# Optimization experiments

Measured on AMD Instinct MI355X. Metric: run time of the kernel, lower is better.

The kernel has to match this reference:

```python
import jax, jax.numpy as jnp
import numpy as np

EMBED = 1024
HEADS = 16
HEAD_DIM = EMBED // HEADS
HIDDEN = 4 * EMBED
EPS = 1e-5


def layer_norm(x, g, b):
    mu = jnp.mean(x, axis=-1, keepdims=True)
    var = jnp.var(x, axis=-1, keepdims=True)
    return (x - mu) * jax.lax.rsqrt(var + EPS) * g + b


def setup_inputs() -> dict:
    key = jax.random.key(0)
    ks = jax.random.split(key, 12)
    s_e = 1.0 / np.sqrt(EMBED)
    s_h = 1.0 / np.sqrt(HIDDEN)
    return {
        "x": jax.random.normal(ks[0], (8, 1024, EMBED), dtype=jnp.float32),
        "ln1_g": jnp.ones((EMBED,), jnp.float32),
        "ln1_b": jnp.zeros((EMBED,), jnp.float32),
        "w_qkv": jax.random.normal(ks[1], (EMBED, 3 * EMBED), jnp.float32) * s_e,
        "b_qkv": jax.random.normal(ks[2], (3 * EMBED,), jnp.float32) * s_e,
        "w_out": jax.random.normal(ks[3], (EMBED, EMBED), jnp.float32) * s_e,
        "b_out": jax.random.normal(ks[4], (EMBED,), jnp.float32) * s_e,
        "ln2_g": jnp.ones((EMBED,), jnp.float32),
        "ln2_b": jnp.zeros((EMBED,), jnp.float32),
        "w_up": jax.random.normal(ks[5], (EMBED, HIDDEN), jnp.float32) * s_e,
        "b_up": jax.random.normal(ks[6], (HIDDEN,), jnp.float32) * s_e,
        "w_down": jax.random.normal(ks[7], (HIDDEN, EMBED), jnp.float32) * s_h,
        "b_down": jax.random.normal(ks[8], (EMBED,), jnp.float32) * s_h,
    }


def reference(x, ln1_g, ln1_b, w_qkv, b_qkv, w_out, b_out,
              ln2_g, ln2_b, w_up, b_up, w_down, b_down):
    B, T, C = x.shape
    # --- attention sub-block ---
    h = layer_norm(x, ln1_g, ln1_b)
    qkv = h @ w_qkv + b_qkv                                   # [B,T,3C]
    q, k, v = jnp.split(qkv, 3, axis=-1)
    def heads(t):  # [B,T,C] -> [B,H,T,D]
        return t.reshape(B, T, HEADS, HEAD_DIM).transpose(0, 2, 1, 3)
    q, k, v = heads(q), heads(k), heads(v)
    scale = HEAD_DIM ** -0.5
    attn = jax.nn.softmax(jnp.einsum('bhqd,bhkd->bhqk', q, k) * scale, axis=-1)
    y = jnp.einsum('bhqk,bhkd->bhqd', attn, v)                # [B,H,T,D]
    y = y.transpose(0, 2, 1, 3).reshape(B, T, C)
    x = x + y @ w_out + b_out
    # --- MLP sub-block ---
    h = layer_norm(x, ln2_g, ln2_b)
    h = jax.nn.relu(h @ w_up + b_up)
    x = x + h @ w_down + b_down
    return x
```

## Files before the change

kernel.cpp:

```cpp
#include <hip/hip_runtime.h>
#include <stdint.h>


typedef __attribute__((ext_vector_type(8))) short short8;
typedef __attribute__((ext_vector_type(4))) short short4v;
typedef __attribute__((ext_vector_type(4))) float floatx4;

#define NROWS 8192

__device__ __forceinline__ unsigned short f2bf(float f) {
    union { float f; unsigned u; } x; x.f = f;
    unsigned r = x.u + 0x7fffu + ((x.u >> 16) & 1u);
    return (unsigned short)(r >> 16);
}
__device__ __forceinline__ float bf2f(unsigned short h) {
    union { unsigned u; float f; } x; x.u = (unsigned)h << 16; return x.f;
}

__device__ __forceinline__ void gl2lds16(const unsigned short* g, unsigned short* l) {
    __builtin_amdgcn_global_load_lds(
        (const __attribute__((address_space(1))) unsigned int*)(uintptr_t)g,
        (__attribute__((address_space(3))) unsigned int*)(unsigned int)(uintptr_t)l,
        16, 0, 0);
}

__global__ __launch_bounds__(256) void prep_kernel(
    const float* __restrict__ w_qkv, const float* __restrict__ w_out,
    const float* __restrict__ w_up, const float* __restrict__ w_down,
    unsigned short* __restrict__ wqkvT, unsigned short* __restrict__ woutT,
    unsigned short* __restrict__ wupT, unsigned short* __restrict__ wdownT,
    const float* __restrict__ x, const float* __restrict__ g,
    const float* __restrict__ b, unsigned short* __restrict__ h1)
{
    int bid = blockIdx.x;
    __shared__ unsigned short tile[32][33];
    __shared__ float rs[4], rs2[4];
    if (bid < 12288) {
        const float* in; unsigned short* out; int K, N, nb, tb;
        if (bid < 3072)      { in = w_qkv;  out = wqkvT;  K = 1024; N = 3072; nb = 96;  tb = bid; }
        else if (bid < 4096) { in = w_out;  out = woutT;  K = 1024; N = 1024; nb = 32;  tb = bid - 3072; }
        else if (bid < 8192) { in = w_up;   out = wupT;   K = 1024; N = 4096; nb = 128; tb = bid - 4096; }
        else                 { in = w_down; out = wdownT; K = 4096; N = 1024; nb = 32;  tb = bid - 8192; }
        int n0 = (tb % nb) * 32, k0 = (tb / nb) * 32;
        int tx = threadIdx.x & 31, ty = threadIdx.x >> 5;
        #pragma unroll
        for (int i = 0; i < 4; ++i)
            tile[ty + i * 8][tx] = f2bf(in[(size_t)(k0 + ty + i * 8) * N + n0 + tx]);
        __syncthreads();
        #pragma unroll
        for (int i = 0; i < 4; ++i)
            out[(size_t)(n0 + ty + i * 8) * K + k0 + tx] = tile[tx][ty + i * 8];
    } else {
        int row = bid - 12288, t = threadIdx.x;
        const float4* xr = (const float4*)(x + (size_t)row * 1024);
        float4 v = xr[t];
        float s  = v.x + v.y + v.z + v.w;
        float s2 = v.x * v.x + v.y * v.y + v.z * v.z + v.w * v.w;
        #pragma unroll
        for (int off = 32; off; off >>= 1) {
            s  += __shfl_xor(s,  off, 64);
            s2 += __shfl_xor(s2, off, 64);
        }
        int w = t >> 6;
        if ((t & 63) == 0) { rs[w] = s; rs2[w] = s2; }
        __syncthreads();
        s  = rs[0] + rs[1] + rs[2] + rs[3];
        s2 = rs2[0] + rs2[1] + rs2[2] + rs2[3];
        float mean = s * (1.0f / 1024.0f);
        float var  = s2 * (1.0f / 1024.0f) - mean * mean;
        float rstd = rsqrtf(var + 1e-5f);
        float4 gv = ((const float4*)g)[t];
        float4 bv = ((const float4*)b)[t];
        ushort4 o;
        o.x = f2bf((v.x - mean) * rstd * gv.x + bv.x);
        o.y = f2bf((v.y - mean) * rstd * gv.y + bv.y);
        o.z = f2bf((v.z - mean) * rstd * gv.z + bv.z);
        o.w = f2bf((v.w - mean) * rstd * gv.w + bv.w);
        ((ushort4*)(h1 + (size_t)row * 1024))[t] = o;
    }
}

__global__ __launch_bounds__(256) void ln_bf16b(
    const unsigned short* __restrict__ x, const float* __restrict__ g,
    const float* __restrict__ b, unsigned short* __restrict__ out)
{
    int row = blockIdx.x, t = threadIdx.x;
    ushort4 hv = ((const ushort4*)(x + (size_t)row * 1024))[t];
    float v0 = bf2f(hv.x), v1 = bf2f(hv.y), v2 = bf2f(hv.z), v3 = bf2f(hv.w);
    float s  = v0 + v1 + v2 + v3;
    float s2 = v0 * v0 + v1 * v1 + v2 * v2 + v3 * v3;
    #pragma unroll
    for (int off = 32; off; off >>= 1) {
        s  += __shfl_xor(s,  off, 64);
        s2 += __shfl_xor(s2, off, 64);
    }
    __shared__ float rs[4], rs2[4];
    int w = t >> 6;
    if ((t & 63) == 0) { rs[w] = s; rs2[w] = s2; }
    __syncthreads();
    s  = rs[0] + rs[1] + rs[2] + rs[3];
    s2 = rs2[0] + rs2[1] + rs2[2] + rs2[3];
    float mean = s * (1.0f / 1024.0f);
    float var  = s2 * (1.0f / 1024.0f) - mean * mean;
    float rstd = rsqrtf(var + 1e-5f);
    float4 gv = ((const float4*)g)[t];
    float4 bv = ((const float4*)b)[t];
    ushort4 o;
    o.x = f2bf((v0 - mean) * rstd * gv.x + bv.x);
    o.y = f2bf((v1 - mean) * rstd * gv.y + bv.y);
    o.z = f2bf((v2 - mean) * rstd * gv.z + bv.z);
    o.w = f2bf((v3 - mean) * rstd * gv.w + bv.w);
    ((ushort4*)(out + (size_t)row * 1024))[t] = o;
}

template <int MODE>
__global__ __launch_bounds__(512, 2) void gemm_8ph(
    const unsigned short* __restrict__ A, const unsigned short* __restrict__ Bt,
    int M, int N, int K,
    const float* __restrict__ bias,
    unsigned short* __restrict__ outB)
{
    int m0 = blockIdx.x * 256, n0 = blockIdx.y * 256;
    int tid = threadIdx.x;
    int w = tid >> 6, l = tid & 63, quad = l >> 4, lr = l & 15;
    int wm = w >> 2, wn = w & 3;

    __shared__ unsigned short As[2][256 * 64];
    __shared__ unsigned short Bs[2][256 * 64];

    floatx4 acc[8][4];
    #pragma unroll
    for (int i = 0; i < 8; ++i)
        #pragma unroll
        for (int j = 0; j < 4; ++j)
            acc[i][j] = (floatx4){0.f, 0.f, 0.f, 0.f};

    int srow = l >> 3;
    int swz  = ((l & 7) ^ srow) * 8;
    int arow1 = (w < 4) ? 16 * w : 128 + 16 * (w - 4);
    const unsigned short* Ag = A  + (size_t)(m0 + arow1 + srow) * K + swz;
    const unsigned short* Bg = Bt + (size_t)(n0 + 16 * w + srow) * K + swz;
    int nt = K >> 6;

    auto SB = [&](unsigned short* dst, int h, int kt) {
        #pragma unroll
        for (int u = 0; u < 2; ++u)
            gl2lds16(Bg + (size_t)(128 * h + 8 * u) * K + kt * 64,
                     &dst[(128 * h + 16 * w + 8 * u) * 64]);
    };
    auto SA1 = [&](unsigned short* dst, int kt) {
        #pragma unroll
        for (int u = 0; u < 2; ++u)
            gl2lds16(Ag + (size_t)(8 * u) * K + kt * 64,
                     &dst[(arow1 + 8 * u) * 64]);
    };
    auto SA2 = [&](unsigned short* dst, int kt) {
        #pragma unroll
        for (int u = 0; u < 2; ++u)
            gl2lds16(Ag + (size_t)(64 + 8 * u) * K + kt * 64,
                     &dst[(arow1 + 64 + 8 * u) * 64]);
    };

    SB(Bs[0], 0, 0); SB(Bs[0], 1, 0); SA1(As[0], 0); SA2(As[0], 0);
    SB(Bs[1], 0, 1); SB(Bs[1], 1, 1); SA1(As[1], 1);
    asm volatile("s_waitcnt vmcnt(6)" ::: "memory");
    __builtin_amdgcn_s_barrier();

    for (int t = 0; t < nt; ++t) {
        int b = t & 1;
        const unsigned short* Asb = As[b];
        const unsigned short* Bsb = Bs[b];
        short8 bfr[4][2];
        #pragma unroll
        for (int p = 0; p < 4; ++p) {
            if (p == 0)      { if (t + 1 < nt) SA2(As[b ^ 1], t + 1); }
            else if (p == 1) { if (t + 2 < nt) SB(Bs[b], 0, t + 2); }
            else if (p == 2) { if (t + 2 < nt) SB(Bs[b], 1, t + 2); }
            else             { if (t + 2 < nt) SA1(As[b], t + 2); }

            if (p == 0) {
                #pragma unroll
                for (int j = 0; j < 4; ++j)
                    #pragma unroll
                    for (int s = 0; s < 2; ++s)
                        bfr[j][s] = *(const short8*)
                            &Bsb[(64 * wn + 16 * j + lr) * 64 +
                                 (((s * 4 + quad) ^ (lr & 7)) * 8)];
            }
            short8 af[2][2];
            #pragma unroll
            for (int i = 0; i < 2; ++i)
                #pragma unroll
                for (int s = 0; s < 2; ++s)
                    af[i][s] = *(const short8*)
                        &Asb[(128 * wm + 32 * p + 16 * i + lr) * 64 +
                             (((s * 4 + quad) ^ (lr & 7)) * 8)];

            __builtin_amdgcn_s_barrier();
            asm volatile("s_waitcnt lgkmcnt(0)" ::: "memory");
            __builtin_amdgcn_s_setprio(1);
            #pragma unroll
            for (int i = 0; i < 2; ++i)
                #pragma unroll
                for (int j = 0; j < 4; ++j) {
                    acc[2 * p + i][j] = __builtin_amdgcn_mfma_f32_16x16x32_bf16(
                        af[i][0], bfr[j][0], acc[2 * p + i][j], 0, 0, 0);
                    acc[2 * p + i][j] = __builtin_amdgcn_mfma_f32_16x16x32_bf16(
                        af[i][1], bfr[j][1], acc[2 * p + i][j], 0, 0, 0);
                }
            __builtin_amdgcn_s_setprio(0);
            if (p == 3) {
                if (t + 2 >= nt) asm volatile("s_waitcnt vmcnt(0)" ::: "memory");
                else             asm volatile("s_waitcnt vmcnt(6)" ::: "memory");
            }
            __builtin_amdgcn_s_barrier();
        }
    }

    #pragma unroll
    for (int mi = 0; mi < 8; ++mi)
        #pragma unroll
        for (int j = 0; j < 4; ++j)
            #pragma unroll
            for (int r = 0; r < 4; ++r) {
                int m = m0 + 128 * wm + 16 * mi + quad * 4 + r;
                int n = n0 + 64 * wn + 16 * j + lr;
                outB[(size_t)m * N + n] = f2bf(fmaxf(acc[mi][j][r] + bias[n], 0.f));
            }
}

template <int MODE>
__global__ __launch_bounds__(512, 2) void gemm_bn128(
    const unsigned short* __restrict__ A, const unsigned short* __restrict__ Bt,
    int M, int N, int K,
    const float* __restrict__ bias,
    const float* __restrict__ residF, const unsigned short* __restrict__ residB,
    float* __restrict__ outF, unsigned short* __restrict__ outB,
    unsigned short* __restrict__ qO, unsigned short* __restrict__ kO,
    unsigned short* __restrict__ vO)
{
    int m0 = blockIdx.x * 256, n0 = blockIdx.y * 128;
    int tid = threadIdx.x;
    int w = tid >> 6, l = tid & 63, quad = l >> 4, lr = l & 15;
    int wm = w >> 1, wn = w & 1;

    __shared__ unsigned short As[2][256 * 64];
    __shared__ unsigned short Bs[2][128 * 64];

    floatx4 acc[4][4];
    #pragma unroll
    for (int i = 0; i < 4; ++i)
        #pragma unroll
        for (int j = 0; j < 4; ++j)
            acc[i][j] = (floatx4){0.f, 0.f, 0.f, 0.f};

    int srow = l >> 3;
    int swz  = ((l & 7) ^ srow) * 8;
    const unsigned short* Ag = A  + (size_t)(m0 + 16 * w + srow) * K + swz;
    const unsigned short* Bg = Bt + (size_t)(n0 + 16 * w + srow) * K + swz;
    int nt = K >> 6;

    auto SB = [&](unsigned short* dst, int kt) {
        #pragma unroll
        for (int u = 0; u < 2; ++u)
            gl2lds16(Bg + (size_t)(8 * u) * K + kt * 64,
                     &dst[(16 * w + 8 * u) * 64]);
    };
    auto SA1 = [&](unsigned short* dst, int kt) {
        #pragma unroll
        for (int u = 0; u < 2; ++u)
            gl2lds16(Ag + (size_t)(8 * u) * K + kt * 64,
                     &dst[(16 * w + 8 * u) * 64]);
    };
    auto SA2 = [&](unsigned short* dst, int kt) {
        #pragma unroll
        for (int u = 0; u < 2; ++u)
            gl2lds16(Ag + (size_t)(128 + 8 * u) * K + kt * 64,
                     &dst[(128 + 16 * w + 8 * u) * 64]);
    };

    SB(Bs[0], 0); SA1(As[0], 0); SA2(As[0], 0);
    SB(Bs[1], 1);
    asm volatile("s_waitcnt vmcnt(2)" ::: "memory");
    __builtin_amdgcn_s_barrier();

    for (int t = 0; t < nt; ++t) {
        int b = t & 1;
        const unsigned short* Asb = As[b];
        const unsigned short* Bsb = Bs[b];
        short8 bfr[4][2];
        #pragma unroll
        for (int p = 0; p < 2; ++p) {
            if (p == 0) { if (t + 1 < nt) { SA1(As[b ^ 1], t + 1); SA2(As[b ^ 1], t + 1); } }
            else        { if (t + 2 < nt) SB(Bs[b], t + 2); }

            if (p == 0) {
                #pragma unroll
                for (int j = 0; j < 4; ++j)
                    #pragma unroll
                    for (int s = 0; s < 2; ++s)
                        bfr[j][s] = *(const short8*)
                            &Bsb[(64 * wn + 16 * j + lr) * 64 +
                                 (((s * 4 + quad) ^ (lr & 7)) * 8)];
            }
            short8 af[2][2];
            #pragma unroll
            for (int i = 0; i < 2; ++i)
                #pragma unroll
                for (int s = 0; s < 2; ++s)
                    af[i][s] = *(const short8*)
                        &Asb[(64 * wm + 32 * p + 16 * i + lr) * 64 +
                             (((s * 4 + quad) ^ (lr & 7)) * 8)];

            __builtin_amdgcn_s_barrier();
            asm volatile("s_waitcnt lgkmcnt(0)" ::: "memory");
            __builtin_amdgcn_s_setprio(1);
            #pragma unroll
            for (int i = 0; i < 2; ++i)
                #pragma unroll
                for (int j = 0; j < 4; ++j) {
                    acc[2 * p + i][j] = __builtin_amdgcn_mfma_f32_16x16x32_bf16(
                        af[i][0], bfr[j][0], acc[2 * p + i][j], 0, 0, 0);
                    acc[2 * p + i][j] = __builtin_amdgcn_mfma_f32_16x16x32_bf16(
                        af[i][1], bfr[j][1], acc[2 * p + i][j], 0, 0, 0);
                }
            __builtin_amdgcn_s_setprio(0);
            if (p == 1) {
                if (t + 2 >= nt) asm volatile("s_waitcnt vmcnt(0)" ::: "memory");
                else             asm volatile("s_waitcnt vmcnt(2)" ::: "memory");
            }
            __builtin_amdgcn_s_barrier();
        }
    }

    if (MODE == 0) {
        int sel = (n0 + 64 * wn) >> 10;
        if (sel < 2) {
            const float qscale = (sel == 0) ? 0.125f : 1.0f;
            unsigned short* dst = (sel == 0) ? qO : kO;
            #pragma unroll
            for (int mi = 0; mi < 4; ++mi)
                #pragma unroll
                for (int j = 0; j < 4; ++j)
                    #pragma unroll
                    for (int r = 0; r < 4; ++r) {
                        int m = m0 + 64 * wm + 16 * mi + quad * 4 + r;
                        int n = n0 + 64 * wn + 16 * j + lr;
                        float c = (acc[mi][j][r] + bias[n]) * qscale;
                        int bb = m >> 10, tt = m & 1023;
                        int cc = n & 1023, hh = cc >> 6, d = cc & 63;
                        dst[(((size_t)(bb * 16 + hh)) * 1024 + tt) * 64 + d] = f2bf(c);
                    }
        } else {
            int bb = m0 >> 10;
            #pragma unroll
            for (int mi = 0; mi < 4; ++mi) {
                int t0 = (m0 & 1023) + 64 * wm + 16 * mi + quad * 4;
                #pragma unroll
                for (int j = 0; j < 4; ++j) {
                    int n = n0 + 64 * wn + 16 * j + lr;
                    int cc = n & 1023, hh = cc >> 6, d = cc & 63;
                    float bn = bias[n];
                    ushort4 pk;
                    pk.x = f2bf(acc[mi][j][0] + bn);
                    pk.y = f2bf(acc[mi][j][1] + bn);
                    pk.z = f2bf(acc[mi][j][2] + bn);
                    pk.w = f2bf(acc[mi][j][3] + bn);
                    *(ushort4*)&vO[((size_t)(bb * 16 + hh) * 64 + d) * 1024 + t0] = pk;
                }
            }
        }
    } else {
        #pragma unroll
        for (int mi = 0; mi < 4; ++mi)
            #pragma unroll
            for (int j = 0; j < 4; ++j)
                #pragma unroll
                for (int r = 0; r < 4; ++r) {
                    int m = m0 + 64 * wm + 16 * mi + quad * 4 + r;
                    int n = n0 + 64 * wn + 16 * j + lr;
                    float c = acc[mi][j][r] + bias[n];
                    if (MODE == 1)
                        outB[(size_t)m * N + n] = f2bf(c + residF[(size_t)m * N + n]);
                    else
                        outF[(size_t)m * N + n] = c + bf2f(residB[(size_t)m * N + n]);
                }
    }
}

__global__ __launch_bounds__(256, 2) void attn_kernel(
    const unsigned short* __restrict__ qg, const unsigned short* __restrict__ kg,
    const unsigned short* __restrict__ vtg, unsigned short* __restrict__ y)
{
    int bid = blockIdx.x;
    int bh = bid & 127, qt = bid >> 7;
    int b = bh >> 4, h = bh & 15;
    int tid = threadIdx.x;
    int w = tid >> 6, l = tid & 63, quad = l >> 4, lr = l & 15;

    __shared__ unsigned short Qs[128 * 64];
    __shared__ unsigned short Ks[2][64 * 64];
    __shared__ unsigned short Vs[2][64 * 64];
    __shared__ unsigned short Ps[4][32 * 68];

    int srow = l >> 3;
    int scol = ((l & 7) ^ srow) * 8;

    {
        const unsigned short* qbase = qg + (size_t)bh * 65536 + (size_t)(qt * 128) * 64;
        #pragma unroll
        for (int u = 0; u < 4; ++u)
            gl2lds16(qbase + (size_t)(32 * w + 8 * u + srow) * 64 + scol,
                     &Qs[(32 * w + 8 * u) * 64]);
    }
    const unsigned short* kbase = kg  + (size_t)bh * 65536;
    const unsigned short* vbase = vtg + (size_t)bh * 65536;

    #pragma unroll
    for (int u = 0; u < 2; ++u) {
        gl2lds16(kbase + (size_t)(16 * w + 8 * u + srow) * 64 + scol,
                 &Ks[0][(16 * w + 8 * u) * 64]);
        gl2lds16(vbase + (size_t)(16 * w + 8 * u + srow) * 1024 + scol,
                 &Vs[0][(16 * w + 8 * u) * 64]);
    }
    __syncthreads();

    short8 af[2][2];
    #pragma unroll
    for (int i = 0; i < 2; ++i)
        #pragma unroll
        for (int s = 0; s < 2; ++s)
            af[i][s] = *(const short8*)
                &Qs[(32 * w + 16 * i + lr) * 64 + ((s * 4 + quad) ^ (lr & 7)) * 8];

    floatx4 o[2][4];
    float lsum[2][4];
    #pragma unroll
    for (int i = 0; i < 2; ++i)
        #pragma unroll
        for (int j = 0; j < 4; ++j) o[i][j] = (floatx4){0.f, 0.f, 0.f, 0.f};
    #pragma unroll
    for (int i = 0; i < 2; ++i)
        #pragma unroll
        for (int r = 0; r < 4; ++r) lsum[i][r] = 0.f;

    for (int kt = 0; kt < 16; ++kt) {
        int cur = kt & 1;
        if (kt + 1 < 16) {
            const unsigned short* kb = kbase + (size_t)((kt + 1) * 64) * 64;
            const unsigned short* vb = vbase + (size_t)((kt + 1) * 64);
            #pragma unroll
            for (int u = 0; u < 2; ++u) {
                gl2lds16(kb + (size_t)(16 * w + 8 * u + srow) * 64 + scol,
                         &Ks[cur ^ 1][(16 * w + 8 * u) * 64]);
                gl2lds16(vb + (size_t)(16 * w + 8 * u + srow) * 1024 + scol,
                         &Vs[cur ^ 1][(16 * w + 8 * u) * 64]);
            }
        }

        short8 kf[4][2];
        #pragma unroll
        for (int j = 0; j < 4; ++j)
            #pragma unroll
            for (int s = 0; s < 2; ++s)
                kf[j][s] = *(const short8*)
                    &Ks[cur][(16 * j + lr) * 64 + ((s * 4 + quad) ^ (lr & 7)) * 8];

        floatx4 s[2][4];
        #pragma unroll
        for (int i = 0; i < 2; ++i)
            #pragma unroll
            for (int j = 0; j < 4; ++j) {
                s[i][j] = (floatx4){0.f, 0.f, 0.f, 0.f};
                #pragma unroll
                for (int st = 0; st < 2; ++st)
                    s[i][j] = __builtin_amdgcn_mfma_f32_16x16x32_bf16(
                        af[i][st], kf[j][st], s[i][j], 0, 0, 0);
            }

        #pragma unroll
        for (int i = 0; i < 2; ++i)
            #pragma unroll
            for (int j = 0; j < 4; ++j)
                #pragma unroll
                for (int r = 0; r < 4; ++r) {
                    float p = __expf(s[i][j][r]);
                    lsum[i][r] += p;
                    Ps[w][(16 * i + quad * 4 + r) * 68 + 16 * j + lr] = f2bf(p);
                }

        asm volatile("s_waitcnt lgkmcnt(0)" ::: "memory");

        short8 vf[4][2];
        #pragma unroll
        for (int j = 0; j < 4; ++j)
            #pragma unroll
            for (int s = 0; s < 2; ++s)
                vf[j][s] = *(const short8*)
                    &Vs[cur][(16 * j + lr) * 64 + ((s * 4 + quad) ^ (lr & 7)) * 8];

        #pragma unroll
        for (int i = 0; i < 2; ++i)
            #pragma unroll
            for (int st = 0; st < 2; ++st) {
                short4v p0 = *(const short4v*)&Ps[w][(16 * i + lr) * 68 + st * 32 + quad * 8];
                short4v p1 = *(const short4v*)&Ps[w][(16 * i + lr) * 68 + st * 32 + quad * 8 + 4];
                short8 pf;
                #pragma unroll
                for (int e = 0; e < 4; ++e) { pf[e] = p0[e]; pf[e + 4] = p1[e]; }
                #pragma unroll
                for (int j = 0; j < 4; ++j)
                    o[i][j] = __builtin_amdgcn_mfma_f32_16x16x32_bf16(
                        pf, vf[j][st], o[i][j], 0, 0, 0);
            }
        __syncthreads();
    }

    #pragma unroll
    for (int off = 8; off; off >>= 1)
        #pragma unroll
        for (int i = 0; i < 2; ++i)
            #pragma unroll
            for (int r = 0; r < 4; ++r)
                lsum[i][r] += __shfl_xor(lsum[i][r], off, 64);
    float rinv[2][4];
    #pragma unroll
    for (int i = 0; i < 2; ++i)
        #pragma unroll
        for (int r = 0; r < 4; ++r) rinv[i][r] = 1.0f / lsum[i][r];

    #pragma unroll
    for (int i = 0; i < 2; ++i)
        #pragma unroll
        for (int j = 0; j < 4; ++j)
            #pragma unroll
            for (int r = 0; r < 4; ++r) {
                int trow = qt * 128 + 32 * w + 16 * i + quad * 4 + r;
                int col  = h * 64 + 16 * j + lr;
                y[((size_t)b * 1024 + trow) * 1024 + col] =
                    f2bf(o[i][j][r] * rinv[i][r]);
            }
}

extern "C" void kernel_launch(void* const* d_in, const int* in_sizes, int n_in,
                              void* d_out, int out_size, void* d_ws, size_t ws_size,
                              hipStream_t stream)
{
    const float* x      = (const float*)d_in[0];
    const float* ln1_g  = (const float*)d_in[1];
    const float* ln1_b  = (const float*)d_in[2];
    const float* w_qkv  = (const float*)d_in[3];
    const float* b_qkv  = (const float*)d_in[4];
    const float* w_out  = (const float*)d_in[5];
    const float* b_out  = (const float*)d_in[6];
    const float* ln2_g  = (const float*)d_in[7];
    const float* ln2_b  = (const float*)d_in[8];
    const float* w_up   = (const float*)d_in[9];
    const float* b_up   = (const float*)d_in[10];
    const float* w_down = (const float*)d_in[11];
    const float* b_down = (const float*)d_in[12];

    char* ws = (char*)d_ws;
    unsigned short* wqkvT  = (unsigned short*)(ws + 0);
    unsigned short* woutT  = (unsigned short*)(ws + 6291456);
    unsigned short* wupT   = (unsigned short*)(ws + 8388608);
    unsigned short* wdownT = (unsigned short*)(ws + 16777216);
    unsigned short* x2     = (unsigned short*)(ws + 25165824);
    unsigned short* h1     = (unsigned short*)(ws + 58720256);
    unsigned short* qb     = (unsigned short*)(ws + 75497472);
    unsigned short* kb     = (unsigned short*)(ws + 92274688);
    unsigned short* vtb    = (unsigned short*)(ws + 109051904);
    unsigned short* yb     = (unsigned short*)(ws + 125829120);
    unsigned short* a2     = (unsigned short*)(ws + 75497472);
    unsigned short* h2     = h1;

    prep_kernel<<<20480, 256, 0, stream>>>(
        w_qkv, w_out, w_up, w_down, wqkvT, woutT, wupT, wdownT,
        x, ln1_g, ln1_b, h1);

    gemm_bn128<0><<<dim3(NROWS / 256, 3072 / 128), 512, 0, stream>>>(
        h1, wqkvT, NROWS, 3072, 1024, b_qkv,
        nullptr, nullptr, nullptr, nullptr, qb, kb, vtb);

    attn_kernel<<<1024, 256, 0, stream>>>(qb, kb, vtb, yb);

    gemm_bn128<1><<<dim3(NROWS / 256, 1024 / 128), 512, 0, stream>>>(
        yb, woutT, NROWS, 1024, 1024, b_out,
        x, nullptr, nullptr, x2, nullptr, nullptr, nullptr);

    ln_bf16b<<<NROWS, 256, 0, stream>>>(x2, ln2_g, ln2_b, h2);

    gemm_8ph<2><<<dim3(NROWS / 256, 4096 / 256), 512, 0, stream>>>(
        h2, wupT, NROWS, 4096, 1024, b_up, a2);

    gemm_bn128<3><<<dim3(NROWS / 256, 1024 / 128), 512, 0, stream>>>(
        a2, wdownT, NROWS, 1024, 4096, b_down,
        nullptr, x2, (float*)d_out, nullptr, nullptr, nullptr, nullptr);
}
```

Baseline: 427.9 us.

## Triple-buffer LDS tiles in bn128 GEMM with one barrier per k-step

```diff
diff --git a/kernel.cpp b/kernel.cpp
--- a/kernel.cpp
+++ b/kernel.cpp
@@ -244,8 +244,8 @@
     int w = tid >> 6, l = tid & 63, quad = l >> 4, lr = l & 15;
     int wm = w >> 1, wn = w & 1;
 
-    __shared__ unsigned short As[2][256 * 64];
-    __shared__ unsigned short Bs[2][128 * 64];
+    __shared__ unsigned short As[3][256 * 64];
+    __shared__ unsigned short Bs[3][128 * 64];
 
     floatx4 acc[4][4];
     #pragma unroll
@@ -260,77 +260,63 @@
     const unsigned short* Bg = Bt + (size_t)(n0 + 16 * w + srow) * K + swz;
     int nt = K >> 6;
 
-    auto SB = [&](unsigned short* dst, int kt) {
+    auto ST = [&](int buf, int kt) {
+        #pragma unroll
+        for (int u = 0; u < 2; ++u)
+            gl2lds16(Ag + (size_t)(8 * u) * K + kt * 64,
+                     &As[buf][(16 * w + 8 * u) * 64]);
+        #pragma unroll
+        for (int u = 0; u < 2; ++u)
+            gl2lds16(Ag + (size_t)(128 + 8 * u) * K + kt * 64,
+                     &As[buf][(128 + 16 * w + 8 * u) * 64]);
         #pragma unroll
         for (int u = 0; u < 2; ++u)
             gl2lds16(Bg + (size_t)(8 * u) * K + kt * 64,
-                     &dst[(16 * w + 8 * u) * 64]);
+                     &Bs[buf][(16 * w + 8 * u) * 64]);
     };
-    auto SA1 = [&](unsigned short* dst, int kt) {
-        #pragma unroll
-        for (int u = 0; u < 2; ++u)
-            gl2lds16(Ag + (size_t)(8 * u) * K + kt * 64,
-                     &dst[(16 * w + 8 * u) * 64]);
-    };
-    auto SA2 = [&](unsigned short* dst, int kt) {
-        #pragma unroll
-        for (int u = 0; u < 2; ++u)
-            gl2lds16(Ag + (size_t)(128 + 8 * u) * K + kt * 64,
-                     &dst[(128 + 16 * w + 8 * u) * 64]);
-    };
-
-    SB(Bs[0], 0); SA1(As[0], 0); SA2(As[0], 0);
-    SB(Bs[1], 1);
-    asm volatile("s_waitcnt vmcnt(2)" ::: "memory");
+
+    ST(0, 0);
+    if (nt > 1) ST(1, 1);
+    asm volatile("s_waitcnt vmcnt(6)" ::: "memory");
     __builtin_amdgcn_s_barrier();
 
+    int cur = 0, pre = 2;
     for (int t = 0; t < nt; ++t) {
-        int b = t & 1;
-        const unsigned short* Asb = As[b];
-        const unsigned short* Bsb = Bs[b];
-        short8 bfr[4][2];
-        #pragma unroll
-        for (int p = 0; p < 2; ++p) {
-            if (p == 0) { if (t + 1 < nt) { SA1(As[b ^ 1], t + 1); SA2(As[b ^ 1], t + 1); } }
-            else        { if (t + 2 < nt) SB(Bs[b], t + 2); }
-
-            if (p == 0) {
-                #pragma unroll
-                for (int j = 0; j < 4; ++j)
-                    #pragma unroll
-                    for (int s = 0; s < 2; ++s)
-                        bfr[j][s] = *(const short8*)
-                            &Bsb[(64 * wn + 16 * j + lr) * 64 +
-                                 (((s * 4 + quad) ^ (lr & 7)) * 8)];
-            }
-            short8 af[2][2];
-            #pragma unroll
-            for (int i = 0; i < 2; ++i)
-                #pragma unroll
-                for (int s = 0; s < 2; ++s)
-                    af[i][s] = *(const short8*)
-                        &Asb[(64 * wm + 32 * p + 16 * i + lr) * 64 +
-                             (((s * 4 + quad) ^ (lr & 7)) * 8)];
-
-            __builtin_amdgcn_s_barrier();
-            asm volatile("s_waitcnt lgkmcnt(0)" ::: "memory");
-            __builtin_amdgcn_s_setprio(1);
-            #pragma unroll
-            for (int i = 0; i < 2; ++i)
-                #pragma unroll
-                for (int j = 0; j < 4; ++j) {
-                    acc[2 * p + i][j] = __builtin_amdgcn_mfma_f32_16x16x32_bf16(
-                        af[i][0], bfr[j][0], acc[2 * p + i][j], 0, 0, 0);
-                    acc[2 * p + i][j] = __builtin_amdgcn_mfma_f32_16x16x32_bf16(
-                        af[i][1], bfr[j][1], acc[2 * p + i][j], 0, 0, 0);
-                }
-            __builtin_amdgcn_s_setprio(0);
-            if (p == 1) {
-                if (t + 2 >= nt) asm volatile("s_waitcnt vmcnt(0)" ::: "memory");
-                else             asm volatile("s_waitcnt vmcnt(2)" ::: "memory");
-            }
-            __builtin_amdgcn_s_barrier();
-        }
+        if (t + 2 < nt) ST(pre, t + 2);
+
+        const unsigned short* Asb = As[cur];
+        const unsigned short* Bsb = Bs[cur];
+        short8 bfr[4][2], af[4][2];
+        #pragma unroll
+        for (int j = 0; j < 4; ++j)
+            #pragma unroll
+            for (int s = 0; s < 2; ++s)
+                bfr[j][s] = *(const short8*)
+                    &Bsb[(64 * wn + 16 * j + lr) * 64 +
+                         (((s * 4 + quad) ^ (lr & 7)) * 8)];
+        #pragma unroll
+        for (int i = 0; i < 4; ++i)
+            #pragma unroll
+            for (int s = 0; s < 2; ++s)
+                af[i][s] = *(const short8*)
+                    &Asb[(64 * wm + 16 * i + lr) * 64 +
+                         (((s * 4 + quad) ^ (lr & 7)) * 8)];
+
+        #pragma unroll
+        for (int i = 0; i < 4; ++i)
+            #pragma unroll
+            for (int j = 0; j < 4; ++j) {
+                acc[i][j] = __builtin_amdgcn_mfma_f32_16x16x32_bf16(
+                    af[i][0], bfr[j][0], acc[i][j], 0, 0, 0);
+                acc[i][j] = __builtin_amdgcn_mfma_f32_16x16x32_bf16(
+                    af[i][1], bfr[j][1], acc[i][j], 0, 0, 0);
+            }
+
+        if (t + 2 >= nt) asm volatile("s_waitcnt vmcnt(0)" ::: "memory");
+        else             asm volatile("s_waitcnt vmcnt(6)" ::: "memory");
+        __builtin_amdgcn_s_barrier();
+        cur = (cur == 2) ? 0 : cur + 1;
+        pre = (pre == 2) ? 0 : pre + 1;
     }
 
     if (MODE == 0) {
```

Result: no change. 433.2 us (+1.2%).

## Load attention Q/K/V fragments directly from global; reorder GEMM prefetch after LDS reads

Applied to the files above, without the earlier changes.

```diff
diff --git a/kernel.cpp b/kernel.cpp
--- a/kernel.cpp
+++ b/kernel.cpp
@@ -173,11 +173,6 @@
         short8 bfr[4][2];
         #pragma unroll
         for (int p = 0; p < 4; ++p) {
-            if (p == 0)      { if (t + 1 < nt) SA2(As[b ^ 1], t + 1); }
-            else if (p == 1) { if (t + 2 < nt) SB(Bs[b], 0, t + 2); }
-            else if (p == 2) { if (t + 2 < nt) SB(Bs[b], 1, t + 2); }
-            else             { if (t + 2 < nt) SA1(As[b], t + 2); }
-
             if (p == 0) {
                 #pragma unroll
                 for (int j = 0; j < 4; ++j)
@@ -195,6 +190,12 @@
                     af[i][s] = *(const short8*)
                         &Asb[(128 * wm + 32 * p + 16 * i + lr) * 64 +
                              (((s * 4 + quad) ^ (lr & 7)) * 8)];
+            if (p == 0) asm volatile("s_waitcnt lgkmcnt(8)" ::: "memory");
+
+            if (p == 0)      { if (t + 1 < nt) SA2(As[b ^ 1], t + 1); }
+            else if (p == 1) { if (t + 2 < nt) SB(Bs[b], 0, t + 2); }
+            else if (p == 2) { if (t + 2 < nt) SB(Bs[b], 1, t + 2); }
+            else             { if (t + 2 < nt) SA1(As[b], t + 2); }
 
             __builtin_amdgcn_s_barrier();
             asm volatile("s_waitcnt lgkmcnt(0)" ::: "memory");
@@ -398,40 +399,19 @@
     int tid = threadIdx.x;
     int w = tid >> 6, l = tid & 63, quad = l >> 4, lr = l & 15;
 
-    __shared__ unsigned short Qs[128 * 64];
-    __shared__ unsigned short Ks[2][64 * 64];
-    __shared__ unsigned short Vs[2][64 * 64];
     __shared__ unsigned short Ps[4][32 * 68];
 
-    int srow = l >> 3;
-    int scol = ((l & 7) ^ srow) * 8;
-
-    {
-        const unsigned short* qbase = qg + (size_t)bh * 65536 + (size_t)(qt * 128) * 64;
-        #pragma unroll
-        for (int u = 0; u < 4; ++u)
-            gl2lds16(qbase + (size_t)(32 * w + 8 * u + srow) * 64 + scol,
-                     &Qs[(32 * w + 8 * u) * 64]);
-    }
+    const unsigned short* qbase = qg + (size_t)bh * 65536 + (size_t)(qt * 128 + 32 * w) * 64;
     const unsigned short* kbase = kg  + (size_t)bh * 65536;
     const unsigned short* vbase = vtg + (size_t)bh * 65536;
 
-    #pragma unroll
-    for (int u = 0; u < 2; ++u) {
-        gl2lds16(kbase + (size_t)(16 * w + 8 * u + srow) * 64 + scol,
-                 &Ks[0][(16 * w + 8 * u) * 64]);
-        gl2lds16(vbase + (size_t)(16 * w + 8 * u + srow) * 1024 + scol,
-                 &Vs[0][(16 * w + 8 * u) * 64]);
-    }
-    __syncthreads();
-
     short8 af[2][2];
     #pragma unroll
     for (int i = 0; i < 2; ++i)
         #pragma unroll
         for (int s = 0; s < 2; ++s)
             af[i][s] = *(const short8*)
-                &Qs[(32 * w + 16 * i + lr) * 64 + ((s * 4 + quad) ^ (lr & 7)) * 8];
+                &qbase[(16 * i + lr) * 64 + (s * 4 + quad) * 8];
 
     floatx4 o[2][4];
     float lsum[2][4];
@@ -445,26 +425,13 @@
         for (int r = 0; r < 4; ++r) lsum[i][r] = 0.f;
 
     for (int kt = 0; kt < 16; ++kt) {
-        int cur = kt & 1;
-        if (kt + 1 < 16) {
-            const unsigned short* kb = kbase + (size_t)((kt + 1) * 64) * 64;
-            const unsigned short* vb = vbase + (size_t)((kt + 1) * 64);
-            #pragma unroll
-            for (int u = 0; u < 2; ++u) {
-                gl2lds16(kb + (size_t)(16 * w + 8 * u + srow) * 64 + scol,
-                         &Ks[cur ^ 1][(16 * w + 8 * u) * 64]);
-                gl2lds16(vb + (size_t)(16 * w + 8 * u + srow) * 1024 + scol,
-                         &Vs[cur ^ 1][(16 * w + 8 * u) * 64]);
-            }
-        }
-
         short8 kf[4][2];
         #pragma unroll
         for (int j = 0; j < 4; ++j)
             #pragma unroll
             for (int s = 0; s < 2; ++s)
                 kf[j][s] = *(const short8*)
-                    &Ks[cur][(16 * j + lr) * 64 + ((s * 4 + quad) ^ (lr & 7)) * 8];
+                    &kbase[(size_t)(kt * 64 + 16 * j + lr) * 64 + (s * 4 + quad) * 8];
 
         floatx4 s[2][4];
         #pragma unroll
@@ -497,7 +464,7 @@
             #pragma unroll
             for (int s = 0; s < 2; ++s)
                 vf[j][s] = *(const short8*)
-                    &Vs[cur][(16 * j + lr) * 64 + ((s * 4 + quad) ^ (lr & 7)) * 8];
+                    &vbase[(size_t)(16 * j + lr) * 1024 + kt * 64 + (s * 4 + quad) * 8];
 
         #pragma unroll
         for (int i = 0; i < 2; ++i)
@@ -513,7 +480,6 @@
                     o[i][j] = __builtin_amdgcn_mfma_f32_16x16x32_bf16(
                         pf, vf[j][st], o[i][j], 0, 0, 0);
             }
-        __syncthreads();
     }
 
     #pragma unroll
```

New measurement: 487.7 us. +14.0%, slower.
